# Optimization experiments

Hardware: AMD Instinct MI355X
Metric: run time of the kernel (lower is better)

## Reference

```python
import jax, jax.numpy as jnp
import numpy as np

N = 50000
E = 800000
D_IN = 128
D_OUT = 128


def setup_inputs() -> dict:
    key = jax.random.key(0)
    k1, k2, k3 = jax.random.split(key, 3)
    seq = jax.random.normal(k1, (N, D_IN), dtype=jnp.float32)
    edge_index = jax.random.randint(k2, (2, E), 0, N, dtype=jnp.int32)
    # Glorot-ish init for the GCNConv linear weight [in, out]
    W = jax.random.normal(k3, (D_IN, D_OUT), dtype=jnp.float32) * (1.0 / np.sqrt(D_IN))
    b = jnp.zeros((D_OUT,), dtype=jnp.float32)
    prelu_w = jnp.full((1,), 0.25, dtype=jnp.float32)
    return {"seq": seq, "edge_index": edge_index, "W": W, "b": b, "prelu_w": prelu_w}


def reference(seq, edge_index, W, b, prelu_w):
    # GCNConv: linear transform, add self-loops, symmetric normalization,
    # scatter-add aggregation, bias; then PReLU activation.
    n = seq.shape[0]
    xW = seq @ W  # [N, D_OUT]

    # add self-loops
    loop = jnp.arange(n, dtype=edge_index.dtype)
    row = jnp.concatenate([edge_index[0], loop])  # source
    col = jnp.concatenate([edge_index[1], loop])  # target

    # degree of target nodes (edge weight = 1)
    deg = jax.ops.segment_sum(jnp.ones_like(col, dtype=xW.dtype), col, num_segments=n)
    dinv = jnp.where(deg > 0, jax.lax.rsqrt(deg), 0.0)
    norm = dinv[row] * dinv[col]  # [E+N]

    msg = xW[row] * norm[:, None]  # gather + scale
    out = jax.ops.segment_sum(msg, col, num_segments=n)  # scatter-add
    out = out + b

    # PReLU with single shared weight
    return jnp.where(out > 0, out, prelu_w[0] * out)
```

## Files before the change

### kernel.cpp

```cpp
#include <hip/hip_runtime.h>

constexpr int D = 128;
constexpr int CAP = 48;
constexpr int DPAD = 16;
constexpr int OVFCAP = 65536;

typedef __attribute__((ext_vector_type(8))) short short8;
typedef __attribute__((ext_vector_type(4))) float f32x4;

__device__ __forceinline__ unsigned short f2bf(float f) {
    unsigned u = __float_as_uint(f);
    u += 0x7fffu + ((u >> 16) & 1u);
    return (unsigned short)(u >> 16);
}

__global__ __launch_bounds__(256) void k_prep(const float* __restrict__ W,
                                              unsigned short* __restrict__ Wf,
                                              uint4* __restrict__ zbase, int zcnt4) {
    int tid = blockIdx.x * 256 + threadIdx.x;
    for (int i = tid; i < zcnt4; i += 16384) zbase[i] = make_uint4(0u, 0u, 0u, 0u);

    int j  = tid & 7;
    int l  = (tid >> 3) & 63;
    int g  = tid >> 9;
    int kc = g >> 3, t = g & 7;
    int k  = kc * 32 + ((l >> 4) * 4) + (j & 3) + ((j >> 2) * 16);
    int c  = t * 16 + (l & 15);
    Wf[tid] = f2bf(W[k * D + c]);
}

__global__ __launch_bounds__(256) void k_place_gemm(
        const int* __restrict__ row, const int* __restrict__ col,
        int* __restrict__ degP, int* __restrict__ slots,
        int* __restrict__ ovfCnt, int2* __restrict__ ovf, int E,
        int gemmBlocks,
        const float* __restrict__ seq, const unsigned short* __restrict__ Wf,
        unsigned short* __restrict__ y16, int n) {
    int b = (int)blockIdx.x;
    int half = b >> 1;
    bool isGemm = ((b & 1) == 0) && (half < gemmBlocks);

    if (!isGemm) {
        int pIdx = (b < 2 * gemmBlocks) ? half : (b - gemmBlocks);
        int t = pIdx * 256 + threadIdx.x;
        int e = 2 * t;
        if (e + 1 < E) {
            unsigned long long cc = __builtin_nontemporal_load((const unsigned long long*)(col + e));
            unsigned long long rr = __builtin_nontemporal_load((const unsigned long long*)(row + e));
            int c0 = (int)(cc & 0xffffffffu), c1 = (int)(cc >> 32);
            int r0 = (int)(rr & 0xffffffffu), r1 = (int)(rr >> 32);
            int p0 = atomicAdd(&degP[(size_t)c0 * DPAD], 1);
            int p1 = atomicAdd(&degP[(size_t)c1 * DPAD], 1);
            if (p0 < CAP) slots[(size_t)c0 * CAP + p0] = r0;
            else { int o = atomicAdd(ovfCnt, 1); if (o < OVFCAP) ovf[o] = make_int2(r0, c0); }
            if (p1 < CAP) slots[(size_t)c1 * CAP + p1] = r1;
            else { int o = atomicAdd(ovfCnt, 1); if (o < OVFCAP) ovf[o] = make_int2(r1, c1); }
        } else if (e < E) {
            int c = col[e];
            int r = row[e];
            int p = atomicAdd(&degP[(size_t)c * DPAD], 1);
            if (p < CAP) slots[(size_t)c * CAP + p] = r;
            else { int o = atomicAdd(ovfCnt, 1); if (o < OVFCAP) ovf[o] = make_int2(r, c); }
        }
        return;
    }

    int w  = threadIdx.x >> 6;
    int l  = threadIdx.x & 63;
    int lr = l & 15;
    int lg = l >> 4;

    int row0 = half * 64;
    int m = row0 + w * 16 + lr;
    if (m >= n) m = n - 1;
    const float* sp = seq + (size_t)m * D;

    f32x4 acc[8];
    #pragma unroll
    for (int t = 0; t < 8; ++t) acc[t] = (f32x4){0.f, 0.f, 0.f, 0.f};

    const short8* WfB = (const short8*)Wf;

    #pragma unroll
    for (int kc = 0; kc < 4; ++kc) {
        int kb = kc * 32 + lg * 4;
        float4 lo = *(const float4*)(sp + kb);
        float4 hi = *(const float4*)(sp + kb + 16);
        short8 a;
        a[0] = (short)f2bf(lo.x); a[1] = (short)f2bf(lo.y);
        a[2] = (short)f2bf(lo.z); a[3] = (short)f2bf(lo.w);
        a[4] = (short)f2bf(hi.x); a[5] = (short)f2bf(hi.y);
        a[6] = (short)f2bf(hi.z); a[7] = (short)f2bf(hi.w);
        #pragma unroll
        for (int t = 0; t < 8; ++t) {
            short8 bf = WfB[(kc * 8 + t) * 64 + l];
            acc[t] = __builtin_amdgcn_mfma_f32_16x16x32_bf16(a, bf, acc[t], 0, 0, 0);
        }
    }

    #pragma unroll
    for (int i = 0; i < 4; ++i) {
        int g = row0 + w * 16 + lg * 4 + i;
        if (g < n) {
            unsigned short* yp = y16 + (size_t)g * D + lr;
            #pragma unroll
            for (int t = 0; t < 8; ++t) yp[t * 16] = f2bf(acc[t][i]);
        }
    }
}

__global__ __launch_bounds__(256) void k_dinv(const int* __restrict__ degP,
                                              float* __restrict__ dinv, int n) {
    int i = blockIdx.x * 256 + threadIdx.x;
    if (i < n) dinv[i] = rsqrtf((float)(degP[(size_t)i * DPAD] + 1));
}

__global__ __launch_bounds__(256) void k_agg(
        const int* __restrict__ slots, const int* __restrict__ degP,
        const float* __restrict__ dinv,
        const int* __restrict__ ovfCnt, const int2* __restrict__ ovf,
        const unsigned short* __restrict__ y16,
        const float* __restrict__ b, const float* __restrict__ pw,
        float* __restrict__ out, int n) {
    int wid = (blockIdx.x * 256 + threadIdx.x) >> 6;
    if (wid >= n) return;
    int lane = threadIdx.x & 63;

    int cntf = degP[(size_t)wid * DPAD];
    int cnt = cntf < CAP ? cntf : CAP;
    float dc = dinv[wid];

    unsigned sv = *(const unsigned*)(y16 + (size_t)wid * D + 2 * lane);
    float ax0 = __uint_as_float(sv << 16) * dc;
    float ay0 = __uint_as_float(sv & 0xffff0000u) * dc;
    float ax1 = 0.f, ay1 = 0.f, ax2 = 0.f, ay2 = 0.f, ax3 = 0.f, ay3 = 0.f;
    float ax4 = 0.f, ay4 = 0.f, ax5 = 0.f, ay5 = 0.f, ax6 = 0.f, ay6 = 0.f;
    float ax7 = 0.f, ay7 = 0.f;

    int my = (lane < cnt) ? slots[(size_t)wid * CAP + lane] : 0;

    int k = 0;
    for (; k + 7 < cnt; k += 8) {
        int r0 = __shfl(my, k);
        int r1 = __shfl(my, k + 1);
        int r2 = __shfl(my, k + 2);
        int r3 = __shfl(my, k + 3);
        int r4 = __shfl(my, k + 4);
        int r5 = __shfl(my, k + 5);
        int r6 = __shfl(my, k + 6);
        int r7 = __shfl(my, k + 7);
        float d0 = dinv[r0]; float d1 = dinv[r1]; float d2 = dinv[r2]; float d3 = dinv[r3];
        float d4 = dinv[r4]; float d5 = dinv[r5]; float d6 = dinv[r6]; float d7 = dinv[r7];
        unsigned v0 = *(const unsigned*)(y16 + (size_t)r0 * D + 2 * lane);
        unsigned v1 = *(const unsigned*)(y16 + (size_t)r1 * D + 2 * lane);
        unsigned v2 = *(const unsigned*)(y16 + (size_t)r2 * D + 2 * lane);
        unsigned v3 = *(const unsigned*)(y16 + (size_t)r3 * D + 2 * lane);
        unsigned v4 = *(const unsigned*)(y16 + (size_t)r4 * D + 2 * lane);
        unsigned v5 = *(const unsigned*)(y16 + (size_t)r5 * D + 2 * lane);
        unsigned v6 = *(const unsigned*)(y16 + (size_t)r6 * D + 2 * lane);
        unsigned v7 = *(const unsigned*)(y16 + (size_t)r7 * D + 2 * lane);
        ax0 = fmaf(__uint_as_float(v0 << 16), d0, ax0); ay0 = fmaf(__uint_as_float(v0 & 0xffff0000u), d0, ay0);
        ax1 = fmaf(__uint_as_float(v1 << 16), d1, ax1); ay1 = fmaf(__uint_as_float(v1 & 0xffff0000u), d1, ay1);
        ax2 = fmaf(__uint_as_float(v2 << 16), d2, ax2); ay2 = fmaf(__uint_as_float(v2 & 0xffff0000u), d2, ay2);
        ax3 = fmaf(__uint_as_float(v3 << 16), d3, ax3); ay3 = fmaf(__uint_as_float(v3 & 0xffff0000u), d3, ay3);
        ax4 = fmaf(__uint_as_float(v4 << 16), d4, ax4); ay4 = fmaf(__uint_as_float(v4 & 0xffff0000u), d4, ay4);
        ax5 = fmaf(__uint_as_float(v5 << 16), d5, ax5); ay5 = fmaf(__uint_as_float(v5 & 0xffff0000u), d5, ay5);
        ax6 = fmaf(__uint_as_float(v6 << 16), d6, ax6); ay6 = fmaf(__uint_as_float(v6 & 0xffff0000u), d6, ay6);
        ax7 = fmaf(__uint_as_float(v7 << 16), d7, ax7); ay7 = fmaf(__uint_as_float(v7 & 0xffff0000u), d7, ay7);
    }
    for (; k < cnt; ++k) {
        int r = __shfl(my, k);
        float dr = dinv[r];
        unsigned v = *(const unsigned*)(y16 + (size_t)r * D + 2 * lane);
        ax0 = fmaf(__uint_as_float(v << 16), dr, ax0);
        ay0 = fmaf(__uint_as_float(v & 0xffff0000u), dr, ay0);
    }

    if (cntf > CAP) {
        int m = *ovfCnt; if (m > OVFCAP) m = OVFCAP;
        for (int j = 0; j < m; ++j) {
            int2 pr = ovf[j];
            if (pr.y == wid) {
                float dr = dinv[pr.x];
                unsigned v = *(const unsigned*)(y16 + (size_t)pr.x * D + 2 * lane);
                ax0 = fmaf(__uint_as_float(v << 16), dr, ax0);
                ay0 = fmaf(__uint_as_float(v & 0xffff0000u), dr, ay0);
            }
        }
    }

    float sx = ((ax0 + ax1) + (ax2 + ax3)) + ((ax4 + ax5) + (ax6 + ax7));
    float sy = ((ay0 + ay1) + (ay2 + ay3)) + ((ay4 + ay5) + (ay6 + ay7));

    float2 bb = *(const float2*)(b + 2 * lane);
    float p = pw[0];
    float vx = sx * dc + bb.x;
    float vy = sy * dc + bb.y;
    vx = vx > 0.f ? vx : p * vx;
    vy = vy > 0.f ? vy : p * vy;
    *(float2*)(out + (size_t)wid * D + 2 * lane) = make_float2(vx, vy);
}

extern "C" void kernel_launch(void* const* d_in, const int* in_sizes, int n_in,
                              void* d_out, int out_size, void* d_ws, size_t ws_size,
                              hipStream_t stream) {
    const float* seq = (const float*)d_in[0];
    const int*   ei  = (const int*)d_in[1];
    const float* W   = (const float*)d_in[2];
    const float* b   = (const float*)d_in[3];
    const float* pw  = (const float*)d_in[4];
    int n = in_sizes[0] / D;
    int E = in_sizes[1] / 2;

    float* out = (float*)d_out;

    auto align = [](size_t x) { return (x + 255) & ~(size_t)255; };
    char* p = (char*)d_ws;
    unsigned short* y16 = (unsigned short*)p; p += align((size_t)n * D * sizeof(unsigned short));
    int*  degP   = (int*)p;   size_t degBytes = align((size_t)n * DPAD * sizeof(int)); p += degBytes;
    int*  ovfCnt = (int*)p;   p += 256;
    int2* ovf    = (int2*)p;  p += align((size_t)OVFCAP * sizeof(int2));
    int*  slots  = (int*)p;   p += align((size_t)n * CAP * sizeof(int));
    unsigned short* Wf = (unsigned short*)p; p += align((size_t)D * D * sizeof(unsigned short));
    float* dinv  = (float*)p; p += align((size_t)n * sizeof(float));

    int zcnt4 = (int)((degBytes + 256) / 16);
    k_prep<<<64, 256, 0, stream>>>(W, Wf, (uint4*)degP, zcnt4);

    int GB = (n + 63) / 64;
    int PB = (E + 511) / 512;
    k_place_gemm<<<GB + PB, 256, 0, stream>>>(
        ei, ei + E, degP, slots, ovfCnt, ovf, E, GB, seq, Wf, y16, n);

    k_dinv<<<(n + 255) / 256, 256, 0, stream>>>(degP, dinv, n);

    k_agg<<<(unsigned)(((long long)n * 64 + 255) / 256), 256, 0, stream>>>(
        slots, degP, dinv, ovfCnt, ovf, y16, b, pw, out, n);
}
```

Measured before the change: 101.2 us.

## Build CSR via two-level bucketed counting sort instead of atomic slot placement

Replaces the per-node global-atomic slot array (fixed capacity with overflow list) with a deterministic two-pass bucketed counting sort. A per-block histogram over 256-node buckets is prefix-scanned, edges are scattered into bucket order, and then each bucket is sorted locally in LDS to produce CSR rows, degrees and dinv. Aggregation then reads contiguous neighbor lists in chunks of 64, with no overflow scan. This removes global atomic contention and the padded degree array, at the cost of extra kernel launches, a scan pass and extra intermediate buffers. The scan assumes at most 1024 partial sums, which limits the supported problem size.

```diff
diff --git a/kernel.cpp b/kernel.cpp
--- a/kernel.cpp
+++ b/kernel.cpp
@@ -1,9 +1,6 @@
 #include <hip/hip_runtime.h>
 
 constexpr int D = 128;
-constexpr int CAP = 48;
-constexpr int DPAD = 16;
-constexpr int OVFCAP = 65536;
 
 typedef __attribute__((ext_vector_type(8))) short short8;
 typedef __attribute__((ext_vector_type(4))) float f32x4;
@@ -14,53 +11,121 @@
     return (unsigned short)(u >> 16);
 }
 
-__global__ __launch_bounds__(256) void k_prep(const float* __restrict__ W,
-                                              unsigned short* __restrict__ Wf,
-                                              uint4* __restrict__ zbase, int zcnt4) {
-    int tid = blockIdx.x * 256 + threadIdx.x;
-    for (int i = tid; i < zcnt4; i += 16384) zbase[i] = make_uint4(0u, 0u, 0u, 0u);
-
-    int j  = tid & 7;
-    int l  = (tid >> 3) & 63;
-    int g  = tid >> 9;
-    int kc = g >> 3, t = g & 7;
-    int k  = kc * 32 + ((l >> 4) * 4) + (j & 3) + ((j >> 2) * 16);
-    int c  = t * 16 + (l & 15);
-    Wf[tid] = f2bf(W[k * D + c]);
-}
-
-__global__ __launch_bounds__(256) void k_place_gemm(
+__global__ __launch_bounds__(256) void k_hist(const int* __restrict__ col,
+                                              int* __restrict__ hist, int E, int NBLK, int NBUCK,
+                                              const float* __restrict__ W,
+                                              unsigned short* __restrict__ Wf) {
+    __shared__ int lh[256];
+    int tid = threadIdx.x, blk = blockIdx.x;
+    lh[tid] = 0;
+    __syncthreads();
+    int e = blk * 256 + tid;
+    if (e < E) atomicAdd(&lh[col[e] >> 8], 1);
+    __syncthreads();
+    if (tid < NBUCK) hist[tid * NBLK + blk] = lh[tid];
+
+    if (blk < 64) {
+        int t2 = blk * 256 + tid;
+        int j  = t2 & 7;
+        int l  = (t2 >> 3) & 63;
+        int g  = t2 >> 9;
+        int kc = g >> 3, t = g & 7;
+        int k  = kc * 32 + ((l >> 4) * 4) + (j & 3) + ((j >> 2) * 16);
+        int c  = t * 16 + (l & 15);
+        Wf[t2] = f2bf(W[k * D + c]);
+    }
+}
+
+__global__ __launch_bounds__(256) void k_scan1(const int* __restrict__ in,
+                                               int* __restrict__ outp,
+                                               int* __restrict__ bsum, int n) {
+    int tid = threadIdx.x;
+    int lane = tid & 63, wv = tid >> 6;
+    int i0 = (blockIdx.x * 256 + tid) * 4;
+    int4 v = {0, 0, 0, 0};
+    if (i0 + 3 < n) {
+        v = *(const int4*)(in + i0);
+    } else {
+        if (i0 < n)     v.x = in[i0];
+        if (i0 + 1 < n) v.y = in[i0 + 1];
+        if (i0 + 2 < n) v.z = in[i0 + 2];
+        if (i0 + 3 < n) v.w = in[i0 + 3];
+    }
+    int tsum = v.x + v.y + v.z + v.w;
+    int x = tsum;
+    #pragma unroll
+    for (int off = 1; off < 64; off <<= 1) {
+        int t = __shfl_up(x, off);
+        if (lane >= off) x += t;
+    }
+    __shared__ int ws[4];
+    if (lane == 63) ws[wv] = x;
+    __syncthreads();
+    int woff = 0;
+    #pragma unroll
+    for (int w = 0; w < 3; ++w) if (w < wv) woff += ws[w];
+    int ex = woff + x - tsum;
+    if (i0 < n)     outp[i0]     = ex;
+    if (i0 + 1 < n) outp[i0 + 1] = ex + v.x;
+    if (i0 + 2 < n) outp[i0 + 2] = ex + v.x + v.y;
+    if (i0 + 3 < n) outp[i0 + 3] = ex + v.x + v.y + v.z;
+    if (tid == 255) bsum[blockIdx.x] = woff + x;
+}
+
+__global__ __launch_bounds__(256) void k_scan2(int* __restrict__ bsum, int nb) {
+    int tid = threadIdx.x;
+    int lane = tid & 63, wv = tid >> 6;
+    int i0 = tid * 4;
+    int v0 = 0, v1 = 0, v2 = 0, v3 = 0;
+    if (i0 < nb)     v0 = bsum[i0];
+    if (i0 + 1 < nb) v1 = bsum[i0 + 1];
+    if (i0 + 2 < nb) v2 = bsum[i0 + 2];
+    if (i0 + 3 < nb) v3 = bsum[i0 + 3];
+    int tsum = v0 + v1 + v2 + v3;
+    int x = tsum;
+    #pragma unroll
+    for (int off = 1; off < 64; off <<= 1) {
+        int t = __shfl_up(x, off);
+        if (lane >= off) x += t;
+    }
+    __shared__ int ws[4];
+    if (lane == 63) ws[wv] = x;
+    __syncthreads();
+    int woff = 0;
+    #pragma unroll
+    for (int w = 0; w < 3; ++w) if (w < wv) woff += ws[w];
+    int ex = woff + x - tsum;
+    if (i0 < nb)     bsum[i0]     = ex;
+    if (i0 + 1 < nb) bsum[i0 + 1] = ex + v0;
+    if (i0 + 2 < nb) bsum[i0 + 2] = ex + v0 + v1;
+    if (i0 + 3 < nb) bsum[i0 + 3] = ex + v0 + v1 + v2;
+}
+
+__global__ __launch_bounds__(256) void k_scatter_gemm(
         const int* __restrict__ row, const int* __restrict__ col,
-        int* __restrict__ degP, int* __restrict__ slots,
-        int* __restrict__ ovfCnt, int2* __restrict__ ovf, int E,
+        const int* __restrict__ scanA, const int* __restrict__ bsum,
+        int2* __restrict__ buf1, int E, int NBLK,
         int gemmBlocks,
         const float* __restrict__ seq, const unsigned short* __restrict__ Wf,
         unsigned short* __restrict__ y16, int n) {
+    __shared__ int scnt[256];
     int b = (int)blockIdx.x;
     int half = b >> 1;
     bool isGemm = ((b & 1) == 0) && (half < gemmBlocks);
 
     if (!isGemm) {
         int pIdx = (b < 2 * gemmBlocks) ? half : (b - gemmBlocks);
-        int t = pIdx * 256 + threadIdx.x;
-        int e = 2 * t;
-        if (e + 1 < E) {
-            unsigned long long cc = __builtin_nontemporal_load((const unsigned long long*)(col + e));
-            unsigned long long rr = __builtin_nontemporal_load((const unsigned long long*)(row + e));
-            int c0 = (int)(cc & 0xffffffffu), c1 = (int)(cc >> 32);
-            int r0 = (int)(rr & 0xffffffffu), r1 = (int)(rr >> 32);
-            int p0 = atomicAdd(&degP[(size_t)c0 * DPAD], 1);
-            int p1 = atomicAdd(&degP[(size_t)c1 * DPAD], 1);
-            if (p0 < CAP) slots[(size_t)c0 * CAP + p0] = r0;
-            else { int o = atomicAdd(ovfCnt, 1); if (o < OVFCAP) ovf[o] = make_int2(r0, c0); }
-            if (p1 < CAP) slots[(size_t)c1 * CAP + p1] = r1;
-            else { int o = atomicAdd(ovfCnt, 1); if (o < OVFCAP) ovf[o] = make_int2(r1, c1); }
-        } else if (e < E) {
+        scnt[threadIdx.x] = 0;
+        __syncthreads();
+        int e = pIdx * 256 + threadIdx.x;
+        if (e < E) {
             int c = col[e];
             int r = row[e];
-            int p = atomicAdd(&degP[(size_t)c * DPAD], 1);
-            if (p < CAP) slots[(size_t)c * CAP + p] = r;
-            else { int o = atomicAdd(ovfCnt, 1); if (o < OVFCAP) ovf[o] = make_int2(r, c); }
+            int bucket = c >> 8;
+            int rank = atomicAdd(&scnt[bucket], 1);
+            int idx = bucket * NBLK + pIdx;
+            int base = scanA[idx] + bsum[idx >> 10];
+            buf1[base + rank] = make_int2(r, c);
         }
         return;
     }
@@ -109,16 +174,62 @@
     }
 }
 
-__global__ __launch_bounds__(256) void k_dinv(const int* __restrict__ degP,
-                                              float* __restrict__ dinv, int n) {
-    int i = blockIdx.x * 256 + threadIdx.x;
-    if (i < n) dinv[i] = rsqrtf((float)(degP[(size_t)i * DPAD] + 1));
+__global__ __launch_bounds__(256) void k_placeB(const int2* __restrict__ buf1,
+                                                const int* __restrict__ scanA,
+                                                const int* __restrict__ bsum,
+                                                int* __restrict__ srow,
+                                                int* __restrict__ gstart,
+                                                int* __restrict__ deg,
+                                                float* __restrict__ dinv,
+                                                int E, int NBLK, int NBUCK, int n) {
+    __shared__ int cnt[256], ns[256], cnt2[256], ws[4];
+    int hb = blockIdx.x, tid = threadIdx.x;
+
+    int i0 = hb * NBLK;
+    int s0 = scanA[i0] + bsum[i0 >> 10];
+    int s1 = E;
+    if (hb + 1 < NBUCK) { int i1 = (hb + 1) * NBLK; s1 = scanA[i1] + bsum[i1 >> 10]; }
+
+    cnt[tid] = 0; cnt2[tid] = 0;
+    __syncthreads();
+    for (int i = s0 + tid; i < s1; i += 256)
+        atomicAdd(&cnt[buf1[i].y & 255], 1);
+    __syncthreads();
+
+    int v = cnt[tid];
+    int lane = tid & 63, wv = tid >> 6;
+    int x = v;
+    #pragma unroll
+    for (int off = 1; off < 64; off <<= 1) {
+        int t = __shfl_up(x, off);
+        if (lane >= off) x += t;
+    }
+    if (lane == 63) ws[wv] = x;
+    __syncthreads();
+    int woff = 0;
+    #pragma unroll
+    for (int w = 0; w < 3; ++w) if (w < wv) woff += ws[w];
+    int excl = woff + x - v;
+    ns[tid] = s0 + excl;
+    int gid = hb * 256 + tid;
+    if (gid < n) {
+        gstart[gid] = s0 + excl;
+        deg[gid] = v;
+        dinv[gid] = rsqrtf((float)(v + 1));
+    }
+    __syncthreads();
+
+    for (int i = s0 + tid; i < s1; i += 256) {
+        int2 rc = buf1[i];
+        int lcl = rc.y & 255;
+        int p = atomicAdd(&cnt2[lcl], 1);
+        srow[ns[lcl] + p] = rc.x;
+    }
 }
 
 __global__ __launch_bounds__(256) void k_agg(
-        const int* __restrict__ slots, const int* __restrict__ degP,
-        const float* __restrict__ dinv,
-        const int* __restrict__ ovfCnt, const int2* __restrict__ ovf,
+        const int* __restrict__ srow, const int* __restrict__ gstart,
+        const int* __restrict__ deg, const float* __restrict__ dinv,
         const unsigned short* __restrict__ y16,
         const float* __restrict__ b, const float* __restrict__ pw,
         float* __restrict__ out, int n) {
@@ -126,8 +237,8 @@
     if (wid >= n) return;
     int lane = threadIdx.x & 63;
 
-    int cntf = degP[(size_t)wid * DPAD];
-    int cnt = cntf < CAP ? cntf : CAP;
+    int cnt = deg[wid];
+    int s = gstart[wid];
     float dc = dinv[wid];
 
     unsigned sv = *(const unsigned*)(y16 + (size_t)wid * D + 2 * lane);
@@ -137,55 +248,44 @@
     float ax4 = 0.f, ay4 = 0.f, ax5 = 0.f, ay5 = 0.f, ax6 = 0.f, ay6 = 0.f;
     float ax7 = 0.f, ay7 = 0.f;
 
-    int my = (lane < cnt) ? slots[(size_t)wid * CAP + lane] : 0;
-
-    int k = 0;
-    for (; k + 7 < cnt; k += 8) {
-        int r0 = __shfl(my, k);
-        int r1 = __shfl(my, k + 1);
-        int r2 = __shfl(my, k + 2);
-        int r3 = __shfl(my, k + 3);
-        int r4 = __shfl(my, k + 4);
-        int r5 = __shfl(my, k + 5);
-        int r6 = __shfl(my, k + 6);
-        int r7 = __shfl(my, k + 7);
-        float d0 = dinv[r0]; float d1 = dinv[r1]; float d2 = dinv[r2]; float d3 = dinv[r3];
-        float d4 = dinv[r4]; float d5 = dinv[r5]; float d6 = dinv[r6]; float d7 = dinv[r7];
-        unsigned v0 = *(const unsigned*)(y16 + (size_t)r0 * D + 2 * lane);
-        unsigned v1 = *(const unsigned*)(y16 + (size_t)r1 * D + 2 * lane);
-        unsigned v2 = *(const unsigned*)(y16 + (size_t)r2 * D + 2 * lane);
-        unsigned v3 = *(const unsigned*)(y16 + (size_t)r3 * D + 2 * lane);
-        unsigned v4 = *(const unsigned*)(y16 + (size_t)r4 * D + 2 * lane);
-        unsigned v5 = *(const unsigned*)(y16 + (size_t)r5 * D + 2 * lane);
-        unsigned v6 = *(const unsigned*)(y16 + (size_t)r6 * D + 2 * lane);
-        unsigned v7 = *(const unsigned*)(y16 + (size_t)r7 * D + 2 * lane);
-        ax0 = fmaf(__uint_as_float(v0 << 16), d0, ax0); ay0 = fmaf(__uint_as_float(v0 & 0xffff0000u), d0, ay0);
-        ax1 = fmaf(__uint_as_float(v1 << 16), d1, ax1); ay1 = fmaf(__uint_as_float(v1 & 0xffff0000u), d1, ay1);
-        ax2 = fmaf(__uint_as_float(v2 << 16), d2, ax2); ay2 = fmaf(__uint_as_float(v2 & 0xffff0000u), d2, ay2);
-        ax3 = fmaf(__uint_as_float(v3 << 16), d3, ax3); ay3 = fmaf(__uint_as_float(v3 & 0xffff0000u), d3, ay3);
-        ax4 = fmaf(__uint_as_float(v4 << 16), d4, ax4); ay4 = fmaf(__uint_as_float(v4 & 0xffff0000u), d4, ay4);
-        ax5 = fmaf(__uint_as_float(v5 << 16), d5, ax5); ay5 = fmaf(__uint_as_float(v5 & 0xffff0000u), d5, ay5);
-        ax6 = fmaf(__uint_as_float(v6 << 16), d6, ax6); ay6 = fmaf(__uint_as_float(v6 & 0xffff0000u), d6, ay6);
-        ax7 = fmaf(__uint_as_float(v7 << 16), d7, ax7); ay7 = fmaf(__uint_as_float(v7 & 0xffff0000u), d7, ay7);
-    }
-    for (; k < cnt; ++k) {
-        int r = __shfl(my, k);
-        float dr = dinv[r];
-        unsigned v = *(const unsigned*)(y16 + (size_t)r * D + 2 * lane);
-        ax0 = fmaf(__uint_as_float(v << 16), dr, ax0);
-        ay0 = fmaf(__uint_as_float(v & 0xffff0000u), dr, ay0);
-    }
-
-    if (cntf > CAP) {
-        int m = *ovfCnt; if (m > OVFCAP) m = OVFCAP;
-        for (int j = 0; j < m; ++j) {
-            int2 pr = ovf[j];
-            if (pr.y == wid) {
-                float dr = dinv[pr.x];
-                unsigned v = *(const unsigned*)(y16 + (size_t)pr.x * D + 2 * lane);
-                ax0 = fmaf(__uint_as_float(v << 16), dr, ax0);
-                ay0 = fmaf(__uint_as_float(v & 0xffff0000u), dr, ay0);
-            }
+    for (int base = 0; base < cnt; base += 64) {
+        int chunk = cnt - base; if (chunk > 64) chunk = 64;
+        int my = (base + lane < cnt) ? srow[s + base + lane] : 0;
+        int k = 0;
+        for (; k + 7 < chunk; k += 8) {
+            int r0 = __shfl(my, k);
+            int r1 = __shfl(my, k + 1);
+            int r2 = __shfl(my, k + 2);
+            int r3 = __shfl(my, k + 3);
+            int r4 = __shfl(my, k + 4);
+            int r5 = __shfl(my, k + 5);
+            int r6 = __shfl(my, k + 6);
+            int r7 = __shfl(my, k + 7);
+            float d0 = dinv[r0]; float d1 = dinv[r1]; float d2 = dinv[r2]; float d3 = dinv[r3];
+            float d4 = dinv[r4]; float d5 = dinv[r5]; float d6 = dinv[r6]; float d7 = dinv[r7];
+            unsigned v0 = *(const unsigned*)(y16 + (size_t)r0 * D + 2 * lane);
+            unsigned v1 = *(const unsigned*)(y16 + (size_t)r1 * D + 2 * lane);
+            unsigned v2 = *(const unsigned*)(y16 + (size_t)r2 * D + 2 * lane);
+            unsigned v3 = *(const unsigned*)(y16 + (size_t)r3 * D + 2 * lane);
+            unsigned v4 = *(const unsigned*)(y16 + (size_t)r4 * D + 2 * lane);
+            unsigned v5 = *(const unsigned*)(y16 + (size_t)r5 * D + 2 * lane);
+            unsigned v6 = *(const unsigned*)(y16 + (size_t)r6 * D + 2 * lane);
+            unsigned v7 = *(const unsigned*)(y16 + (size_t)r7 * D + 2 * lane);
+            ax0 = fmaf(__uint_as_float(v0 << 16), d0, ax0); ay0 = fmaf(__uint_as_float(v0 & 0xffff0000u), d0, ay0);
+            ax1 = fmaf(__uint_as_float(v1 << 16), d1, ax1); ay1 = fmaf(__uint_as_float(v1 & 0xffff0000u), d1, ay1);
+            ax2 = fmaf(__uint_as_float(v2 << 16), d2, ax2); ay2 = fmaf(__uint_as_float(v2 & 0xffff0000u), d2, ay2);
+            ax3 = fmaf(__uint_as_float(v3 << 16), d3, ax3); ay3 = fmaf(__uint_as_float(v3 & 0xffff0000u), d3, ay3);
+            ax4 = fmaf(__uint_as_float(v4 << 16), d4, ax4); ay4 = fmaf(__uint_as_float(v4 & 0xffff0000u), d4, ay4);
+            ax5 = fmaf(__uint_as_float(v5 << 16), d5, ax5); ay5 = fmaf(__uint_as_float(v5 & 0xffff0000u), d5, ay5);
+            ax6 = fmaf(__uint_as_float(v6 << 16), d6, ax6); ay6 = fmaf(__uint_as_float(v6 & 0xffff0000u), d6, ay6);
+            ax7 = fmaf(__uint_as_float(v7 << 16), d7, ax7); ay7 = fmaf(__uint_as_float(v7 & 0xffff0000u), d7, ay7);
+        }
+        for (; k < chunk; ++k) {
+            int r = __shfl(my, k);
+            float dr = dinv[r];
+            unsigned vv = *(const unsigned*)(y16 + (size_t)r * D + 2 * lane);
+            ax0 = fmaf(__uint_as_float(vv << 16), dr, ax0);
+            ay0 = fmaf(__uint_as_float(vv & 0xffff0000u), dr, ay0);
         }
     }
 
@@ -214,26 +314,36 @@
 
     float* out = (float*)d_out;
 
+    int NBLK  = (E + 255) / 256;
+    int NBUCK = (n + 255) / 256;
+    int tot   = NBUCK * NBLK;
+    int GB    = (n + 63) / 64;
+
     auto align = [](size_t x) { return (x + 255) & ~(size_t)255; };
     char* p = (char*)d_ws;
     unsigned short* y16 = (unsigned short*)p; p += align((size_t)n * D * sizeof(unsigned short));
-    int*  degP   = (int*)p;   size_t degBytes = align((size_t)n * DPAD * sizeof(int)); p += degBytes;
-    int*  ovfCnt = (int*)p;   p += 256;
-    int2* ovf    = (int2*)p;  p += align((size_t)OVFCAP * sizeof(int2));
-    int*  slots  = (int*)p;   p += align((size_t)n * CAP * sizeof(int));
-    unsigned short* Wf = (unsigned short*)p; p += align((size_t)D * D * sizeof(unsigned short));
-    float* dinv  = (float*)p; p += align((size_t)n * sizeof(float));
-
-    int zcnt4 = (int)((degBytes + 256) / 16);
-    k_prep<<<64, 256, 0, stream>>>(W, Wf, (uint4*)degP, zcnt4);
-
-    int GB = (n + 63) / 64;
-    int PB = (E + 511) / 512;
-    k_place_gemm<<<GB + PB, 256, 0, stream>>>(
-        ei, ei + E, degP, slots, ovfCnt, ovf, E, GB, seq, Wf, y16, n);
-
-    k_dinv<<<(n + 255) / 256, 256, 0, stream>>>(degP, dinv, n);
+    unsigned short* Wf  = (unsigned short*)p; p += align((size_t)D * D * sizeof(unsigned short));
+    int2* buf1  = (int2*)p;  p += align((size_t)E * sizeof(int2));
+    int*  hist  = (int*)p;   p += align((size_t)tot * sizeof(int));
+    int*  scanA = (int*)p;   p += align((size_t)tot * sizeof(int));
+    int*  bsum  = (int*)p;   p += align(1024 * sizeof(int));
+    int*  srow  = (int*)p;   p += align((size_t)E * sizeof(int));
+    int*  gstart= (int*)p;   p += align((size_t)n * sizeof(int));
+    int*  deg   = (int*)p;   p += align((size_t)n * sizeof(int));
+    float* dinv = (float*)p; p += align((size_t)n * sizeof(float));
+
+    k_hist<<<NBLK, 256, 0, stream>>>(ei + E, hist, E, NBLK, NBUCK, W, Wf);
+
+    int sb = (tot + 1023) / 1024;
+    k_scan1<<<sb, 256, 0, stream>>>(hist, scanA, bsum, tot);
+    k_scan2<<<1, 256, 0, stream>>>(bsum, sb);
+
+    k_scatter_gemm<<<GB + NBLK, 256, 0, stream>>>(
+        ei, ei + E, scanA, bsum, buf1, E, NBLK, GB, seq, Wf, y16, n);
+
+    k_placeB<<<NBUCK, 256, 0, stream>>>(buf1, scanA, bsum, srow, gstart, deg, dinv,
+                                        E, NBLK, NBUCK, n);
 
     k_agg<<<(unsigned)(((long long)n * 64 + 255) / 256), 256, 0, stream>>>(
-        slots, degP, dinv, ovfCnt, ovf, y16, b, pw, out, n);
-}
+        srow, gstart, deg, dinv, y16, b, pw, out, n);
+}
```

Measured after the change: 93.32 us. 7.8% less time.
